# Performance work log

Measured on AMD Instinct MI355X. Metric: run time of the kernel, lower is better.

## Reference

```python
import jax, jax.numpy as jnp
import numpy as np
import math

D_MODEL = 1024
NHEAD = 16
D_K = D_MODEL // NHEAD
B, S = 2, 2048


def setup_inputs() -> dict:
    key = jax.random.key(0)
    ks = jax.random.split(key, 9)
    x = jax.random.normal(ks[0], (B, S, D_MODEL), dtype=jnp.float32)
    # causal mask, broadcastable to (B, nhead, S, S); 0 entries are masked out
    mask = jnp.tril(jnp.ones((S, S), dtype=jnp.int32))[None, None, :, :]
    scale = 1.0 / math.sqrt(D_MODEL)
    def lin(kw, kb):
        W = jax.random.uniform(kw, (D_MODEL, D_MODEL), dtype=jnp.float32, minval=-scale, maxval=scale)
        b = jax.random.uniform(kb, (D_MODEL,), dtype=jnp.float32, minval=-scale, maxval=scale)
        return W, b
    Wq, bq = lin(ks[1], ks[2])
    Wk, bk = lin(ks[3], ks[4])
    Wv, bv = lin(ks[5], ks[6])
    Wo, bo = lin(ks[7], ks[8])
    return {"x": x, "mask": mask, "Wq": Wq, "bq": bq, "Wk": Wk, "bk": bk,
            "Wv": Wv, "bv": bv, "Wo": Wo, "bo": bo}


def reference(x, mask, Wq, bq, Wk, bk, Wv, bv, Wo, bo):
    b, s, _ = x.shape
    def heads(W, bias):
        # (b, s, d_model) @ (d_model, d_model) -> (b, nhead, s, d_k)
        return (x @ W.T + bias).reshape(b, s, NHEAD, D_K).transpose(0, 2, 1, 3)
    Q, K, V = heads(Wq, bq), heads(Wk, bk), heads(Wv, bv)
    scores = jnp.einsum('bhqd,bhkd->bhqk', Q, K) / math.sqrt(D_K)
    scores = jnp.where(mask == 0, jnp.float32(-1e9), scores)
    attn = jax.nn.softmax(scores, axis=-1)  # dropout is identity in eval mode
    out = jnp.einsum('bhqk,bhkd->bhqd', attn, V)
    out = out.transpose(0, 2, 1, 3).reshape(b, s, D_MODEL)
    return out @ Wo.T + bo
```

## Files before the change

kernel.cpp:

```cpp
#include <hip/hip_runtime.h>
#include <hip/hip_bf16.h>

#define DMODEL 1024
#define NH     16
#define DKH    64
#define BSZ    2
#define SEQ    2048
#define MROWS  (BSZ*SEQ)
#define WELEM  (DMODEL*DMODEL)

typedef __attribute__((ext_vector_type(8))) short short8;
typedef __attribute__((ext_vector_type(4))) float f32x4;

__device__ __forceinline__ ushort f2bf(float f) {
    return __bfloat16_as_ushort(__float2bfloat16(f));
}
__device__ __forceinline__ unsigned pk2(float lo, float hi) {
    return (unsigned)f2bf(lo) | ((unsigned)f2bf(hi) << 16);
}
__device__ __forceinline__ void load_lds16(const ushort* g, ushort* l) {
    __builtin_amdgcn_global_load_lds(
        (const __attribute__((address_space(1))) unsigned int*)g,
        (__attribute__((address_space(3))) unsigned int*)l, 16, 0, 0);
}

__global__ __launch_bounds__(256)
void cvt_all(const float* __restrict__ x,
             const float* __restrict__ W0, const float* __restrict__ W1,
             const float* __restrict__ W2, const float* __restrict__ W3,
             ushort* __restrict__ xbf, ushort* __restrict__ Wcat,
             ushort* __restrict__ Wo)
{
    const int blk = blockIdx.x;
    const float* src;
    ushort* dst;
    int base;
    if (blk < 2048)      { src = x;  dst = xbf;             base = blk * 2048; }
    else if (blk < 2560) { src = W0; dst = Wcat;            base = (blk - 2048) * 2048; }
    else if (blk < 3072) { src = W1; dst = Wcat + WELEM;    base = (blk - 2560) * 2048; }
    else if (blk < 3584) { src = W2; dst = Wcat + 2*WELEM;  base = (blk - 3072) * 2048; }
    else                 { src = W3; dst = Wo;              base = (blk - 3584) * 2048; }
    const size_t off = (size_t)base + threadIdx.x * 8;
    const float4 f0 = *(const float4*)(src + off);
    const float4 f1 = *(const float4*)(src + off + 4);
    uint4 o;
    o.x = pk2(f0.x, f0.y); o.y = pk2(f0.z, f0.w);
    o.z = pk2(f1.x, f1.y); o.w = pk2(f1.z, f1.w);
    *(uint4*)(dst + off) = o;
}

__global__ __launch_bounds__(256)
void gemm_qkv(const ushort* __restrict__ xbf, const ushort* __restrict__ Wcat,
              const float* __restrict__ bq, const float* __restrict__ bk,
              const float* __restrict__ bv,
              ushort* __restrict__ Qh, ushort* __restrict__ Kh,
              ushort* __restrict__ VT)
{
    __shared__ ushort Ash[128][32];
    __shared__ ushort Bsh[128][32];

    const int t    = threadIdx.x;
    const int m0   = blockIdx.y * 128, n0 = blockIdx.x * 128;
    const int wave = t >> 6;
    const int lane = t & 63;
    const int wr   = (wave >> 1) * 64;
    const int wc   = (wave & 1) * 64;
    const int quad = lane >> 4;
    const int r16  = lane & 15;

    const int row0 = wave * 16 + (lane >> 2);
    const int row1 = 64 + wave * 16 + (lane >> 2);
    const int ch   = (lane & 3) * 8;

    f32x4 acc[4][4];
    #pragma unroll
    for (int i = 0; i < 4; ++i)
        #pragma unroll
        for (int j = 0; j < 4; ++j)
            acc[i][j] = (f32x4){0.f, 0.f, 0.f, 0.f};

    for (int k0 = 0; k0 < DMODEL; k0 += 32) {
        load_lds16(xbf  + (size_t)(m0 + row0) * DMODEL + k0 + ch, &Ash[wave * 16][0]);
        load_lds16(xbf  + (size_t)(m0 + row1) * DMODEL + k0 + ch, &Ash[64 + wave * 16][0]);
        load_lds16(Wcat + (size_t)(n0 + row0) * DMODEL + k0 + ch, &Bsh[wave * 16][0]);
        load_lds16(Wcat + (size_t)(n0 + row1) * DMODEL + k0 + ch, &Bsh[64 + wave * 16][0]);
        __syncthreads();

        short8 af[4], bf[4];
        #pragma unroll
        for (int i = 0; i < 4; ++i) af[i] = *(const short8*)&Ash[wr + i * 16 + r16][quad * 8];
        #pragma unroll
        for (int j = 0; j < 4; ++j) bf[j] = *(const short8*)&Bsh[wc + j * 16 + r16][quad * 8];

        #pragma unroll
        for (int i = 0; i < 4; ++i)
            #pragma unroll
            for (int j = 0; j < 4; ++j)
                acc[i][j] = __builtin_amdgcn_mfma_f32_16x16x32_bf16(af[i], bf[j], acc[i][j], 0, 0, 0);
        __syncthreads();
    }

    const int region = n0 >> 10;
    const float* bp  = (region == 0) ? bq : (region == 1) ? bk : bv;
    ushort* outQK    = (region == 0) ? Qh : Kh;
    const float osc  = (region == 0) ? 0.125f : 1.0f;
    const int nbase  = n0 & 1023;

    #pragma unroll
    for (int i = 0; i < 4; ++i) {
        #pragma unroll
        for (int j = 0; j < 4; ++j) {
            #pragma unroll
            for (int reg = 0; reg < 4; ++reg) {
                const int m  = m0 + wr + i * 16 + quad * 4 + reg;
                const int n  = nbase + wc + j * 16 + r16;
                const float v = (acc[i][j][reg] + bp[n]) * osc;
                const int b = m >> 11, s = m & (SEQ - 1);
                const int h = n >> 6,  dk = n & 63;
                if (region < 2) {
                    outQK[((size_t)(b * NH + h) * SEQ + s) * DKH + dk] = f2bf(v);
                } else {
                    VT[(((size_t)(b * NH + h)) * DKH + dk) * SEQ + s] = f2bf(v);
                }
            }
        }
    }
}

__global__ __launch_bounds__(256)
void gemm_out(const ushort* __restrict__ O, const ushort* __restrict__ Wo,
              const float* __restrict__ bo, float* __restrict__ out)
{
    __shared__ ushort Ash[128][32];
    __shared__ ushort Bsh[64][32];

    const int t    = threadIdx.x;
    const int m0   = blockIdx.y * 128, n0 = blockIdx.x * 64;
    const int wave = t >> 6;
    const int lane = t & 63;
    const int wr   = (wave >> 1) * 64;
    const int wc   = (wave & 1) * 32;
    const int quad = lane >> 4;
    const int r16  = lane & 15;

    const int row0 = wave * 16 + (lane >> 2);
    const int row1 = 64 + wave * 16 + (lane >> 2);
    const int ch   = (lane & 3) * 8;

    f32x4 acc[4][2];
    #pragma unroll
    for (int i = 0; i < 4; ++i)
        #pragma unroll
        for (int j = 0; j < 2; ++j)
            acc[i][j] = (f32x4){0.f, 0.f, 0.f, 0.f};

    for (int k0 = 0; k0 < DMODEL; k0 += 32) {
        const int ma0 = m0 + row0, ma1 = m0 + row1;
        load_lds16(O + ((size_t)(ma0 >> 11) * NH + (k0 >> 6)) * (SEQ * DKH)
                     + (size_t)(ma0 & (SEQ - 1)) * DKH + (k0 & 63) + ch,
                   &Ash[wave * 16][0]);
        load_lds16(O + ((size_t)(ma1 >> 11) * NH + (k0 >> 6)) * (SEQ * DKH)
                     + (size_t)(ma1 & (SEQ - 1)) * DKH + (k0 & 63) + ch,
                   &Ash[64 + wave * 16][0]);
        load_lds16(Wo + (size_t)(n0 + row0) * DMODEL + k0 + ch, &Bsh[wave * 16][0]);
        __syncthreads();

        short8 af[4], bf[2];
        #pragma unroll
        for (int i = 0; i < 4; ++i) af[i] = *(const short8*)&Ash[wr + i * 16 + r16][quad * 8];
        #pragma unroll
        for (int j = 0; j < 2; ++j) bf[j] = *(const short8*)&Bsh[wc + j * 16 + r16][quad * 8];

        #pragma unroll
        for (int i = 0; i < 4; ++i)
            #pragma unroll
            for (int j = 0; j < 2; ++j)
                acc[i][j] = __builtin_amdgcn_mfma_f32_16x16x32_bf16(af[i], bf[j], acc[i][j], 0, 0, 0);
        __syncthreads();
    }

    #pragma unroll
    for (int i = 0; i < 4; ++i) {
        #pragma unroll
        for (int j = 0; j < 2; ++j) {
            #pragma unroll
            for (int reg = 0; reg < 4; ++reg) {
                const int m = m0 + wr + i * 16 + quad * 4 + reg;
                const int n = n0 + wc + j * 16 + r16;
                out[(size_t)m * DMODEL + n] = acc[i][j][reg] + bo[n];
            }
        }
    }
}

__global__ __launch_bounds__(256)
void gemm_mfma(const void* __restrict__ A, const void* __restrict__ W,
               const float* __restrict__ bias, void* __restrict__ out,
               int amode, int bmode, int outmode, float oscale)
{
    __shared__ ushort Ash[128][40];
    __shared__ ushort Bsh[128][40];

    const int t    = threadIdx.x;
    const int m0   = blockIdx.y * 128, n0 = blockIdx.x * 128;
    const int srow = t >> 1;
    const int shal = (t & 1) * 16;

    const int wave = t >> 6;
    const int lane = t & 63;
    const int wr   = (wave >> 1) * 64;
    const int wc   = (wave & 1) * 64;
    const int quad = lane >> 4;
    const int r16  = lane & 15;

    f32x4 acc[4][4];
    #pragma unroll
    for (int i = 0; i < 4; ++i)
        #pragma unroll
        for (int j = 0; j < 4; ++j)
            acc[i][j] = (f32x4){0.f, 0.f, 0.f, 0.f};

    for (int k0 = 0; k0 < DMODEL; k0 += 32) {
        uint4 a01, a23, b01, b23;
        if (amode == 0) {
            const float* ap = (const float*)A + (size_t)(m0 + srow) * DMODEL + k0 + shal;
            const float4 f0 = *(const float4*)(ap);
            const float4 f1 = *(const float4*)(ap + 4);
            const float4 f2 = *(const float4*)(ap + 8);
            const float4 f3 = *(const float4*)(ap + 12);
            a01 = (uint4){pk2(f0.x,f0.y), pk2(f0.z,f0.w), pk2(f1.x,f1.y), pk2(f1.z,f1.w)};
            a23 = (uint4){pk2(f2.x,f2.y), pk2(f2.z,f2.w), pk2(f3.x,f3.y), pk2(f3.z,f3.w)};
        } else if (amode == 1) {
            const int m = m0 + srow;
            const ushort* ap = (const ushort*)A
                + ((size_t)(m >> 11) * NH + (k0 >> 6)) * (SEQ * DKH)
                + (size_t)(m & (SEQ - 1)) * DKH + (k0 & 63) + shal;
            a01 = *(const uint4*)(ap);
            a23 = *(const uint4*)(ap + 8);
        } else {
            const ushort* ap = (const ushort*)A + (size_t)(m0 + srow) * DMODEL + k0 + shal;
            a01 = *(const uint4*)(ap);
            a23 = *(const uint4*)(ap + 8);
        }
        if (bmode == 0) {
            const float* wp = (const float*)W + (size_t)(n0 + srow) * DMODEL + k0 + shal;
            const float4 w0 = *(const float4*)(wp);
            const float4 w1 = *(const float4*)(wp + 4);
            const float4 w2 = *(const float4*)(wp + 8);
            const float4 w3 = *(const float4*)(wp + 12);
            b01 = (uint4){pk2(w0.x,w0.y), pk2(w0.z,w0.w), pk2(w1.x,w1.y), pk2(w1.z,w1.w)};
            b23 = (uint4){pk2(w2.x,w2.y), pk2(w2.z,w2.w), pk2(w3.x,w3.y), pk2(w3.z,w3.w)};
        } else {
            const ushort* wp = (const ushort*)W + (size_t)(n0 + srow) * DMODEL + k0 + shal;
            b01 = *(const uint4*)(wp);
            b23 = *(const uint4*)(wp + 8);
        }

        *(uint4*)&Ash[srow][shal]     = a01;
        *(uint4*)&Ash[srow][shal + 8] = a23;
        *(uint4*)&Bsh[srow][shal]     = b01;
        *(uint4*)&Bsh[srow][shal + 8] = b23;
        __syncthreads();

        short8 af[4], bf[4];
        #pragma unroll
        for (int i = 0; i < 4; ++i) af[i] = *(const short8*)&Ash[wr + i * 16 + r16][quad * 8];
        #pragma unroll
        for (int j = 0; j < 4; ++j) bf[j] = *(const short8*)&Bsh[wc + j * 16 + r16][quad * 8];

        #pragma unroll
        for (int i = 0; i < 4; ++i)
            #pragma unroll
            for (int j = 0; j < 4; ++j)
                acc[i][j] = __builtin_amdgcn_mfma_f32_16x16x32_bf16(af[i], bf[j], acc[i][j], 0, 0, 0);
        __syncthreads();
    }

    #pragma unroll
    for (int i = 0; i < 4; ++i) {
        #pragma unroll
        for (int j = 0; j < 4; ++j) {
            #pragma unroll
            for (int reg = 0; reg < 4; ++reg) {
                const int m = m0 + wr + i * 16 + quad * 4 + reg;
                const int n = n0 + wc + j * 16 + r16;
                const float v = (acc[i][j][reg] + bias[n]) * oscale;
                if (outmode == 0) {
                    ((float*)out)[(size_t)m * DMODEL + n] = v;
                } else if (outmode == 1) {
                    ((ushort*)out)[((size_t)(m >> 11) * NH + (n >> 6)) * (SEQ * DKH)
                                   + (size_t)(m & (SEQ - 1)) * DKH + (n & 63)] = f2bf(v);
                } else {
                    ((ushort*)out)[(((size_t)(m >> 11) * NH + (n >> 6)) * DKH + (n & 63)) * SEQ
                                   + (m & (SEQ - 1))] = f2bf(v);
                }
            }
        }
    }
}

__global__ __launch_bounds__(256)
void attn_flash(ushort* __restrict__ Qh,
                const ushort* __restrict__ Kh,
                const ushort* __restrict__ VT)
{
    __shared__ ushort Kl[128][72];
    __shared__ ushort Vl[64][136];
    __shared__ ushort Pl[4][16][136];

    const int t256 = threadIdx.x;
    const int wave = t256 >> 6;
    const int lane = t256 & 63;
    const int quad = lane >> 4;
    const int r16  = lane & 15;

    const int slot = blockIdx.x & 7;
    const int bh   = slot * 4 + ((blockIdx.x >> 3) & 3);
    const int qt   = blockIdx.x >> 5;
    const int q0   = qt * 64;

    ushort*       Qbase = Qh + (size_t)bh * SEQ * DKH;
    const ushort* Kbase = Kh + (size_t)bh * SEQ * DKH;
    const ushort* Vbase = VT + (size_t)bh * DKH * SEQ;

    short8 qf[2];
    {
        const ushort* qrow = Qbase + (size_t)(q0 + wave * 16 + r16) * DKH;
        qf[0] = *(const short8*)(qrow + quad * 8);
        qf[1] = *(const short8*)(qrow + 32 + quad * 8);
    }

    f32x4 oacc[4];
    #pragma unroll
    for (int i = 0; i < 4; ++i) oacc[i] = (f32x4){0.f, 0.f, 0.f, 0.f};
    float lpart[4] = {0.f, 0.f, 0.f, 0.f};

    const int T   = (qt >> 1) + 1;
    const int off = (qt & 1) * 64;

    for (int t = 0; t < T; ++t) {
        {
            const int krow = t256 >> 1, kc = (t256 & 1) * 32;
            const ushort* kg = Kbase + (size_t)(t * 128 + krow) * DKH + kc;
            *(uint4*)&Kl[krow][kc]      = *(const uint4*)(kg);
            *(uint4*)&Kl[krow][kc + 8]  = *(const uint4*)(kg + 8);
            *(uint4*)&Kl[krow][kc + 16] = *(const uint4*)(kg + 16);
            *(uint4*)&Kl[krow][kc + 24] = *(const uint4*)(kg + 24);
            const int vrow = t256 >> 2, vc = (t256 & 3) * 32;
            const ushort* vg = Vbase + (size_t)vrow * SEQ + t * 128 + vc;
            *(uint4*)&Vl[vrow][vc]      = *(const uint4*)(vg);
            *(uint4*)&Vl[vrow][vc + 8]  = *(const uint4*)(vg + 8);
            *(uint4*)&Vl[vrow][vc + 16] = *(const uint4*)(vg + 16);
            *(uint4*)&Vl[vrow][vc + 24] = *(const uint4*)(vg + 24);
        }
        __syncthreads();

        f32x4 sacc[8];
        #pragma unroll
        for (int nt = 0; nt < 8; ++nt) {
            sacc[nt] = (f32x4){0.f, 0.f, 0.f, 0.f};
            short8 b0 = *(const short8*)&Kl[nt * 16 + r16][quad * 8];
            short8 b1 = *(const short8*)&Kl[nt * 16 + r16][32 + quad * 8];
            sacc[nt] = __builtin_amdgcn_mfma_f32_16x16x32_bf16(qf[0], b0, sacc[nt], 0, 0, 0);
            sacc[nt] = __builtin_amdgcn_mfma_f32_16x16x32_bf16(qf[1], b1, sacc[nt], 0, 0, 0);
        }

        const bool diag = (t == T - 1);
        #pragma unroll
        for (int reg = 0; reg < 4; ++reg) {
            const int row_local = wave * 16 + quad * 4 + reg + off;
            #pragma unroll
            for (int nt = 0; nt < 8; ++nt) {
                float pv = __expf(sacc[nt][reg]);
                if (diag && (nt * 16 + r16) > row_local) pv = 0.f;
                lpart[reg] += pv;
                Pl[wave][quad * 4 + reg][nt * 16 + r16] = f2bf(pv);
            }
        }

        #pragma unroll
        for (int c = 0; c < 4; ++c) {
            short8 af = *(const short8*)&Pl[wave][r16][c * 32 + quad * 8];
            #pragma unroll
            for (int ct = 0; ct < 4; ++ct) {
                short8 bf = *(const short8*)&Vl[ct * 16 + r16][c * 32 + quad * 8];
                oacc[ct] = __builtin_amdgcn_mfma_f32_16x16x32_bf16(af, bf, oacc[ct], 0, 0, 0);
            }
        }
        __syncthreads();
    }

    #pragma unroll
    for (int reg = 0; reg < 4; ++reg)
        for (int d = 1; d < 16; d <<= 1)
            lpart[reg] += __shfl_xor(lpart[reg], d, 64);

    #pragma unroll
    for (int reg = 0; reg < 4; ++reg) {
        const float inv = 1.f / lpart[reg];
        const int q = q0 + wave * 16 + quad * 4 + reg;
        ushort* orow = Qbase + (size_t)q * DKH;
        #pragma unroll
        for (int ct = 0; ct < 4; ++ct)
            orow[ct * 16 + r16] = f2bf(oacc[ct][reg] * inv);
    }
}

extern "C" void kernel_launch(void* const* d_in, const int* in_sizes, int n_in,
                              void* d_out, int out_size, void* d_ws, size_t ws_size,
                              hipStream_t stream)
{
    const float* x  = (const float*)d_in[0];
    const float* Wf[4] = {(const float*)d_in[2], (const float*)d_in[4],
                          (const float*)d_in[6], (const float*)d_in[8]};
    const float* Bf[4] = {(const float*)d_in[3], (const float*)d_in[5],
                          (const float*)d_in[7], (const float*)d_in[9]};

    const size_t HSZ = (size_t)MROWS * DMODEL;
    ushort* Qh = (ushort*)d_ws;
    ushort* Kh = (ushort*)d_out;
    ushort* VT = (ushort*)d_out + HSZ;

    const dim3 blk(256);

    if (ws_size >= 24u * 1024 * 1024) {
        ushort* Wcat = Qh + HSZ;
        ushort* Wo   = Wcat + 3 * (size_t)WELEM;
        ushort* xbf  = Wo + WELEM;

        cvt_all<<<dim3(4096), blk, 0, stream>>>(x, Wf[0], Wf[1], Wf[2], Wf[3],
                                                xbf, Wcat, Wo);

        gemm_qkv<<<dim3(3 * DMODEL / 128, MROWS / 128), blk, 0, stream>>>(
            xbf, Wcat, Bf[0], Bf[1], Bf[2], Qh, Kh, VT);

        attn_flash<<<dim3(BSZ * NH * 32), blk, 0, stream>>>(Qh, Kh, VT);

        gemm_out<<<dim3(DMODEL / 64, MROWS / 128), blk, 0, stream>>>(
            Qh, Wo, Bf[3], (float*)d_out);
    } else {
        const dim3 gg(DMODEL / 128, MROWS / 128);
        gemm_mfma<<<gg, blk, 0, stream>>>(x, Wf[0], Bf[0], Qh, 0, 0, 1, 0.125f);
        gemm_mfma<<<gg, blk, 0, stream>>>(x, Wf[1], Bf[1], Kh, 0, 0, 1, 1.0f);
        gemm_mfma<<<gg, blk, 0, stream>>>(x, Wf[2], Bf[2], VT, 0, 0, 2, 1.0f);
        attn_flash<<<dim3(BSZ * NH * 32), blk, 0, stream>>>(Qh, Kh, VT);
        gemm_mfma<<<gg, blk, 0, stream>>>(Qh, Wf[3], Bf[3], d_out, 1, 0, 0, 1.0f);
    }
}
```

Before: 214.1 us.

## Pair causal query tiles per attention block and deepen GEMM K-step to 64

Each attention block now processes two query tiles (p and 31-p), so every block does roughly the same amount of causal work and the grid is halved. This removes the load imbalance where late query tiles took many more key steps than early ones. The QKV and output GEMMs now load two 32-wide K slices per barrier, halving the number of synchronisations per tile in exchange for doubling LDS use. Halving the grid to 512 blocks may leave some compute units underused.

After: 227.8 us. +6.4%, slower.

```diff
diff --git a/kernel.cpp b/kernel.cpp
--- a/kernel.cpp
+++ b/kernel.cpp
@@ -56,8 +56,8 @@
               ushort* __restrict__ Qh, ushort* __restrict__ Kh,
               ushort* __restrict__ VT)
 {
-    __shared__ ushort Ash[128][32];
-    __shared__ ushort Bsh[128][32];
+    __shared__ ushort Ash[2][128][32];
+    __shared__ ushort Bsh[2][128][32];
 
     const int t    = threadIdx.x;
     const int m0   = blockIdx.y * 128, n0 = blockIdx.x * 128;
@@ -79,24 +79,30 @@
         for (int j = 0; j < 4; ++j)
             acc[i][j] = (f32x4){0.f, 0.f, 0.f, 0.f};
 
-    for (int k0 = 0; k0 < DMODEL; k0 += 32) {
-        load_lds16(xbf  + (size_t)(m0 + row0) * DMODEL + k0 + ch, &Ash[wave * 16][0]);
-        load_lds16(xbf  + (size_t)(m0 + row1) * DMODEL + k0 + ch, &Ash[64 + wave * 16][0]);
-        load_lds16(Wcat + (size_t)(n0 + row0) * DMODEL + k0 + ch, &Bsh[wave * 16][0]);
-        load_lds16(Wcat + (size_t)(n0 + row1) * DMODEL + k0 + ch, &Bsh[64 + wave * 16][0]);
-        __syncthreads();
-
-        short8 af[4], bf[4];
-        #pragma unroll
-        for (int i = 0; i < 4; ++i) af[i] = *(const short8*)&Ash[wr + i * 16 + r16][quad * 8];
-        #pragma unroll
-        for (int j = 0; j < 4; ++j) bf[j] = *(const short8*)&Bsh[wc + j * 16 + r16][quad * 8];
-
-        #pragma unroll
-        for (int i = 0; i < 4; ++i)
-            #pragma unroll
-            for (int j = 0; j < 4; ++j)
-                acc[i][j] = __builtin_amdgcn_mfma_f32_16x16x32_bf16(af[i], bf[j], acc[i][j], 0, 0, 0);
+    for (int k0 = 0; k0 < DMODEL; k0 += 64) {
+        #pragma unroll
+        for (int s = 0; s < 2; ++s) {
+            const int kc = k0 + s * 32;
+            load_lds16(xbf  + (size_t)(m0 + row0) * DMODEL + kc + ch, &Ash[s][wave * 16][0]);
+            load_lds16(xbf  + (size_t)(m0 + row1) * DMODEL + kc + ch, &Ash[s][64 + wave * 16][0]);
+            load_lds16(Wcat + (size_t)(n0 + row0) * DMODEL + kc + ch, &Bsh[s][wave * 16][0]);
+            load_lds16(Wcat + (size_t)(n0 + row1) * DMODEL + kc + ch, &Bsh[s][64 + wave * 16][0]);
+        }
+        __syncthreads();
+
+        #pragma unroll
+        for (int s = 0; s < 2; ++s) {
+            short8 af[4], bf[4];
+            #pragma unroll
+            for (int i = 0; i < 4; ++i) af[i] = *(const short8*)&Ash[s][wr + i * 16 + r16][quad * 8];
+            #pragma unroll
+            for (int j = 0; j < 4; ++j) bf[j] = *(const short8*)&Bsh[s][wc + j * 16 + r16][quad * 8];
+            #pragma unroll
+            for (int i = 0; i < 4; ++i)
+                #pragma unroll
+                for (int j = 0; j < 4; ++j)
+                    acc[i][j] = __builtin_amdgcn_mfma_f32_16x16x32_bf16(af[i], bf[j], acc[i][j], 0, 0, 0);
+        }
         __syncthreads();
     }
 
@@ -131,8 +137,8 @@
 void gemm_out(const ushort* __restrict__ O, const ushort* __restrict__ Wo,
               const float* __restrict__ bo, float* __restrict__ out)
 {
-    __shared__ ushort Ash[128][32];
-    __shared__ ushort Bsh[64][32];
+    __shared__ ushort Ash[2][128][32];
+    __shared__ ushort Bsh[2][64][32];
 
     const int t    = threadIdx.x;
     const int m0   = blockIdx.y * 128, n0 = blockIdx.x * 64;
@@ -154,28 +160,34 @@
         for (int j = 0; j < 2; ++j)
             acc[i][j] = (f32x4){0.f, 0.f, 0.f, 0.f};
 
-    for (int k0 = 0; k0 < DMODEL; k0 += 32) {
-        const int ma0 = m0 + row0, ma1 = m0 + row1;
-        load_lds16(O + ((size_t)(ma0 >> 11) * NH + (k0 >> 6)) * (SEQ * DKH)
-                     + (size_t)(ma0 & (SEQ - 1)) * DKH + (k0 & 63) + ch,
-                   &Ash[wave * 16][0]);
-        load_lds16(O + ((size_t)(ma1 >> 11) * NH + (k0 >> 6)) * (SEQ * DKH)
-                     + (size_t)(ma1 & (SEQ - 1)) * DKH + (k0 & 63) + ch,
-                   &Ash[64 + wave * 16][0]);
-        load_lds16(Wo + (size_t)(n0 + row0) * DMODEL + k0 + ch, &Bsh[wave * 16][0]);
-        __syncthreads();
-
-        short8 af[4], bf[2];
-        #pragma unroll
-        for (int i = 0; i < 4; ++i) af[i] = *(const short8*)&Ash[wr + i * 16 + r16][quad * 8];
-        #pragma unroll
-        for (int j = 0; j < 2; ++j) bf[j] = *(const short8*)&Bsh[wc + j * 16 + r16][quad * 8];
-
-        #pragma unroll
-        for (int i = 0; i < 4; ++i)
-            #pragma unroll
-            for (int j = 0; j < 2; ++j)
-                acc[i][j] = __builtin_amdgcn_mfma_f32_16x16x32_bf16(af[i], bf[j], acc[i][j], 0, 0, 0);
+    for (int k0 = 0; k0 < DMODEL; k0 += 64) {
+        #pragma unroll
+        for (int s = 0; s < 2; ++s) {
+            const int kc = k0 + s * 32;
+            const int ma0 = m0 + row0, ma1 = m0 + row1;
+            load_lds16(O + ((size_t)(ma0 >> 11) * NH + (kc >> 6)) * (SEQ * DKH)
+                         + (size_t)(ma0 & (SEQ - 1)) * DKH + (kc & 63) + ch,
+                       &Ash[s][wave * 16][0]);
+            load_lds16(O + ((size_t)(ma1 >> 11) * NH + (kc >> 6)) * (SEQ * DKH)
+                         + (size_t)(ma1 & (SEQ - 1)) * DKH + (kc & 63) + ch,
+                       &Ash[s][64 + wave * 16][0]);
+            load_lds16(Wo + (size_t)(n0 + row0) * DMODEL + kc + ch, &Bsh[s][wave * 16][0]);
+        }
+        __syncthreads();
+
+        #pragma unroll
+        for (int s = 0; s < 2; ++s) {
+            short8 af[4], bf[2];
+            #pragma unroll
+            for (int i = 0; i < 4; ++i) af[i] = *(const short8*)&Ash[s][wr + i * 16 + r16][quad * 8];
+            #pragma unroll
+            for (int j = 0; j < 2; ++j) bf[j] = *(const short8*)&Bsh[s][wc + j * 16 + r16][quad * 8];
+            #pragma unroll
+            for (int i = 0; i < 4; ++i)
+                #pragma unroll
+                for (int j = 0; j < 2; ++j)
+                    acc[i][j] = __builtin_amdgcn_mfma_f32_16x16x32_bf16(af[i], bf[j], acc[i][j], 0, 0, 0);
+        }
         __syncthreads();
     }
 
@@ -315,94 +327,101 @@
     const int r16  = lane & 15;
 
     const int slot = blockIdx.x & 7;
-    const int bh   = slot * 4 + ((blockIdx.x >> 3) & 3);
-    const int qt   = blockIdx.x >> 5;
-    const int q0   = qt * 64;
+    const int rest = blockIdx.x >> 3;
+    const int bh   = slot * 4 + (rest & 3);
+    const int p    = rest >> 2;
 
     ushort*       Qbase = Qh + (size_t)bh * SEQ * DKH;
     const ushort* Kbase = Kh + (size_t)bh * SEQ * DKH;
     const ushort* Vbase = VT + (size_t)bh * DKH * SEQ;
 
-    short8 qf[2];
-    {
-        const ushort* qrow = Qbase + (size_t)(q0 + wave * 16 + r16) * DKH;
-        qf[0] = *(const short8*)(qrow + quad * 8);
-        qf[1] = *(const short8*)(qrow + 32 + quad * 8);
-    }
-
-    f32x4 oacc[4];
-    #pragma unroll
-    for (int i = 0; i < 4; ++i) oacc[i] = (f32x4){0.f, 0.f, 0.f, 0.f};
-    float lpart[4] = {0.f, 0.f, 0.f, 0.f};
-
-    const int T   = (qt >> 1) + 1;
-    const int off = (qt & 1) * 64;
-
-    for (int t = 0; t < T; ++t) {
+    #pragma unroll
+    for (int pass = 0; pass < 2; ++pass) {
+        const int qt = pass ? (31 - p) : p;
+        const int q0 = qt * 64;
+
+        short8 qf[2];
         {
-            const int krow = t256 >> 1, kc = (t256 & 1) * 32;
-            const ushort* kg = Kbase + (size_t)(t * 128 + krow) * DKH + kc;
-            *(uint4*)&Kl[krow][kc]      = *(const uint4*)(kg);
-            *(uint4*)&Kl[krow][kc + 8]  = *(const uint4*)(kg + 8);
-            *(uint4*)&Kl[krow][kc + 16] = *(const uint4*)(kg + 16);
-            *(uint4*)&Kl[krow][kc + 24] = *(const uint4*)(kg + 24);
-            const int vrow = t256 >> 2, vc = (t256 & 3) * 32;
-            const ushort* vg = Vbase + (size_t)vrow * SEQ + t * 128 + vc;
-            *(uint4*)&Vl[vrow][vc]      = *(const uint4*)(vg);
-            *(uint4*)&Vl[vrow][vc + 8]  = *(const uint4*)(vg + 8);
-            *(uint4*)&Vl[vrow][vc + 16] = *(const uint4*)(vg + 16);
-            *(uint4*)&Vl[vrow][vc + 24] = *(const uint4*)(vg + 24);
-        }
-        __syncthreads();
-
-        f32x4 sacc[8];
-        #pragma unroll
-        for (int nt = 0; nt < 8; ++nt) {
-            sacc[nt] = (f32x4){0.f, 0.f, 0.f, 0.f};
-            short8 b0 = *(const short8*)&Kl[nt * 16 + r16][quad * 8];
-            short8 b1 = *(const short8*)&Kl[nt * 16 + r16][32 + quad * 8];
-            sacc[nt] = __builtin_amdgcn_mfma_f32_16x16x32_bf16(qf[0], b0, sacc[nt], 0, 0, 0);
-            sacc[nt] = __builtin_amdgcn_mfma_f32_16x16x32_bf16(qf[1], b1, sacc[nt], 0, 0, 0);
-        }
-
-        const bool diag = (t == T - 1);
+            const ushort* qrow = Qbase + (size_t)(q0 + wave * 16 + r16) * DKH;
+            qf[0] = *(const short8*)(qrow + quad * 8);
+            qf[1] = *(const short8*)(qrow + 32 + quad * 8);
+        }
+
+        f32x4 oacc[4];
+        #pragma unroll
+        for (int i = 0; i < 4; ++i) oacc[i] = (f32x4){0.f, 0.f, 0.f, 0.f};
+        float lpart[4] = {0.f, 0.f, 0.f, 0.f};
+
+        const int T   = (qt >> 1) + 1;
+        const int off = (qt & 1) * 64;
+
+        for (int t = 0; t < T; ++t) {
+            {
+                const int krow = t256 >> 1, kc = (t256 & 1) * 32;
+                const ushort* kg = Kbase + (size_t)(t * 128 + krow) * DKH + kc;
+                *(uint4*)&Kl[krow][kc]      = *(const uint4*)(kg);
+                *(uint4*)&Kl[krow][kc + 8]  = *(const uint4*)(kg + 8);
+                *(uint4*)&Kl[krow][kc + 16] = *(const uint4*)(kg + 16);
+                *(uint4*)&Kl[krow][kc + 24] = *(const uint4*)(kg + 24);
+                const int vrow = t256 >> 2, vc = (t256 & 3) * 32;
+                const ushort* vg = Vbase + (size_t)vrow * SEQ + t * 128 + vc;
+                *(uint4*)&Vl[vrow][vc]      = *(const uint4*)(vg);
+                *(uint4*)&Vl[vrow][vc + 8]  = *(const uint4*)(vg + 8);
+                *(uint4*)&Vl[vrow][vc + 16] = *(const uint4*)(vg + 16);
+                *(uint4*)&Vl[vrow][vc + 24] = *(const uint4*)(vg + 24);
+            }
+            __syncthreads();
+
+            f32x4 sacc[8];
+            #pragma unroll
+            for (int nt = 0; nt < 8; ++nt) {
+                sacc[nt] = (f32x4){0.f, 0.f, 0.f, 0.f};
+                short8 b0 = *(const short8*)&Kl[nt * 16 + r16][quad * 8];
+                short8 b1 = *(const short8*)&Kl[nt * 16 + r16][32 + quad * 8];
+                sacc[nt] = __builtin_amdgcn_mfma_f32_16x16x32_bf16(qf[0], b0, sacc[nt], 0, 0, 0);
+                sacc[nt] = __builtin_amdgcn_mfma_f32_16x16x32_bf16(qf[1], b1, sacc[nt], 0, 0, 0);
+            }
+
+            const bool diag = (t == T - 1);
+            #pragma unroll
+            for (int reg = 0; reg < 4; ++reg) {
+                const int row_local = wave * 16 + quad * 4 + reg + off;
+                #pragma unroll
+                for (int nt = 0; nt < 8; ++nt) {
+                    float pv = __expf(sacc[nt][reg]);
+                    if (diag && (nt * 16 + r16) > row_local) pv = 0.f;
+                    lpart[reg] += pv;
+                    Pl[wave][quad * 4 + reg][nt * 16 + r16] = f2bf(pv);
+                }
+            }
+
+            #pragma unroll
+            for (int c = 0; c < 4; ++c) {
+                short8 af = *(const short8*)&Pl[wave][r16][c * 32 + quad * 8];
+                #pragma unroll
+                for (int ct = 0; ct < 4; ++ct) {
+                    short8 bf = *(const short8*)&Vl[ct * 16 + r16][c * 32 + quad * 8];
+                    oacc[ct] = __builtin_amdgcn_mfma_f32_16x16x32_bf16(af, bf, oacc[ct], 0, 0, 0);
+                }
+            }
+            __syncthreads();
+        }
+
+        #pragma unroll
+        for (int reg = 0; reg < 4; ++reg)
+            for (int d = 1; d < 16; d <<= 1)
+                lpart[reg] += __shfl_xor(lpart[reg], d, 64);
+
         #pragma unroll
         for (int reg = 0; reg < 4; ++reg) {
-            const int row_local = wave * 16 + quad * 4 + reg + off;
-            #pragma unroll
-            for (int nt = 0; nt < 8; ++nt) {
-                float pv = __expf(sacc[nt][reg]);
-                if (diag && (nt * 16 + r16) > row_local) pv = 0.f;
-                lpart[reg] += pv;
-                Pl[wave][quad * 4 + reg][nt * 16 + r16] = f2bf(pv);
-            }
-        }
-
-        #pragma unroll
-        for (int c = 0; c < 4; ++c) {
-            short8 af = *(const short8*)&Pl[wave][r16][c * 32 + quad * 8];
-            #pragma unroll
-            for (int ct = 0; ct < 4; ++ct) {
-                short8 bf = *(const short8*)&Vl[ct * 16 + r16][c * 32 + quad * 8];
-                oacc[ct] = __builtin_amdgcn_mfma_f32_16x16x32_bf16(af, bf, oacc[ct], 0, 0, 0);
-            }
-        }
-        __syncthreads();
-    }
-
-    #pragma unroll
-    for (int reg = 0; reg < 4; ++reg)
-        for (int d = 1; d < 16; d <<= 1)
-            lpart[reg] += __shfl_xor(lpart[reg], d, 64);
-
-    #pragma unroll
-    for (int reg = 0; reg < 4; ++reg) {
-        const float inv = 1.f / lpart[reg];
-        const int q = q0 + wave * 16 + quad * 4 + reg;
-        ushort* orow = Qbase + (size_t)q * DKH;
-        #pragma unroll
-        for (int ct = 0; ct < 4; ++ct)
-            orow[ct * 16 + r16] = f2bf(oacc[ct][reg] * inv);
+            const float inv = 1.f / lpart[reg];
+            const int q = q0 + wave * 16 + quad * 4 + reg;
+            ushort* orow = Qbase + (size_t)q * DKH;
+            #pragma unroll
+            for (int ct = 0; ct < 4; ++ct)
+                orow[ct * 16 + r16] = f2bf(oacc[ct][reg] * inv);
+        }
+        __syncthreads();
     }
 }
 
@@ -434,7 +453,7 @@
         gemm_qkv<<<dim3(3 * DMODEL / 128, MROWS / 128), blk, 0, stream>>>(
             xbf, Wcat, Bf[0], Bf[1], Bf[2], Qh, Kh, VT);
 
-        attn_flash<<<dim3(BSZ * NH * 32), blk, 0, stream>>>(Qh, Kh, VT);
+        attn_flash<<<dim3(BSZ * NH * 16), blk, 0, stream>>>(Qh, Kh, VT);
 
         gemm_out<<<dim3(DMODEL / 64, MROWS / 128), blk, 0, stream>>>(
             Qh, Wo, Bf[3], (float*)d_out);
@@ -443,7 +462,7 @@
         gemm_mfma<<<gg, blk, 0, stream>>>(x, Wf[0], Bf[0], Qh, 0, 0, 1, 0.125f);
         gemm_mfma<<<gg, blk, 0, stream>>>(x, Wf[1], Bf[1], Kh, 0, 0, 1, 1.0f);
         gemm_mfma<<<gg, blk, 0, stream>>>(x, Wf[2], Bf[2], VT, 0, 0, 2, 1.0f);
-        attn_flash<<<dim3(BSZ * NH * 32), blk, 0, stream>>>(Qh, Kh, VT);
+        attn_flash<<<dim3(BSZ * NH * 16), blk, 0, stream>>>(Qh, Kh, VT);
         gemm_mfma<<<gg, blk, 0, stream>>>(Qh, Wf[3], Bf[3], d_out, 1, 0, 0, 1.0f);
     }
 }
```
